# Kernel optimization log

Hardware: AMD Instinct MI355X
Metric: run time of the kernel (lower is better)

Reference implementation:

```python
import jax, jax.numpy as jnp
import numpy as np

B, N, K = 4, 1024, 4          # batch, nodes, neighbors-per-side (degree 2K)
FN, FE = 128, 64              # input node/edge feature dims
CN, CE = 128, 64              # output node/edge channels


def _build_graph():
    # degree-8 circulant graph; fixed edge count E = N*K
    A = np.zeros((N, N), np.float32)
    for d in range(1, K + 1):
        i = np.arange(N)
        A[i, (i + d) % N] = 1.0
        A[(i + d) % N, i] = 1.0
    # incidence matrix from upper-triangular nonzeros (row-major, as torch.nonzero)
    r, c = np.nonzero(np.triu(A))
    E = r.shape[0]
    inc = np.zeros((N, E), np.float32)
    ar = np.arange(E)
    inc[r, ar] = 1.0
    inc[c, ar] = 1.0

    def gcn_filter(M):
        Mh = M + np.eye(M.shape[0], dtype=np.float32)
        deg = Mh.sum(1)
        deg[deg == 0] = 1.0
        di = deg ** -0.5
        return (Mh * di[:, None]) * di[None, :]

    lap = gcn_filter(A)                                   # node GCN filter [N,N]
    line_adj = inc.T @ inc - 2.0 * np.eye(E, dtype=np.float32)  # line graph [E,E]
    edge_lap = gcn_filter(line_adj)                       # edge GCN filter [E,E]
    return lap, edge_lap, inc, E


def setup_inputs() -> dict:
    lap, edge_lap, inc, E = _build_graph()
    key = jax.random.key(0)
    ks = jax.random.split(key, 8)
    tile = lambda m: jnp.broadcast_to(jnp.asarray(m), (B,) + m.shape)
    return {
        "x": jax.random.normal(ks[0], (B, N, FN), jnp.float32),
        "e": jax.random.normal(ks[1], (B, E, FE), jnp.float32),
        "laplacian": tile(lap),
        "edge_laplacian": tile(edge_lap),
        "incidence": tile(inc),
        "node_kernel": jax.random.normal(ks[2], (FN, CN), jnp.float32) / np.sqrt(FN).astype(np.float32),
        "edge_kernel": jax.random.normal(ks[3], (FE, CE), jnp.float32) / np.sqrt(FE).astype(np.float32),
        "node_weights": jax.random.normal(ks[4], (FN, 1), jnp.float32) * 0.1,
        "edge_weights": jax.random.normal(ks[5], (FE, 1), jnp.float32) * 0.1,
        "node_bias": jax.random.uniform(ks[6], (CN,), jnp.float32, -0.05, 0.05),
        "edge_bias": jax.random.uniform(ks[7], (CE,), jnp.float32, -0.05, 0.05),
    }


def reference(x, e, laplacian, edge_laplacian, incidence, node_kernel, edge_kernel,
              node_weights, edge_weights, node_bias, edge_bias):
    # ---- node propagation: T diag(e @ ew) T^T * L_node, then @ x @ Wn ----
    we = jnp.einsum('bef,fo->be', e, edge_weights)  # [B,E], squeezed edge scores
    # incidence @ diag(we) @ incidence^T  == (incidence * we) @ incidence^T
    node_adj = jnp.matmul(incidence * we[:, None, :],
                          jnp.swapaxes(incidence, -1, -2)) * laplacian  # [B,N,N]
    node_out = jnp.matmul(jnp.matmul(node_adj, x), node_kernel) + node_bias
    node_out = jax.nn.relu(node_out)  # [B,N,CN]

    # ---- edge propagation: T^T diag(x @ nw) T * L_edge, then @ e @ We ----
    wn = jnp.einsum('bnf,fo->bn', x, node_weights)  # [B,N]
    inc_t = jnp.swapaxes(incidence, -1, -2)         # [B,E,N]
    edge_adj = jnp.matmul(inc_t * wn[:, None, :], incidence) * edge_laplacian  # [B,E,E]
    edge_out = jnp.matmul(jnp.matmul(edge_adj, e), edge_kernel) + edge_bias
    edge_out = jax.nn.relu(edge_out)  # [B,E,CE]

    return node_out, edge_out
```

## Files before the change

### kernel.cpp

```cpp
#include <hip/hip_runtime.h>

#define BB   4
#define NN   1024
#define EE   4096
#define FN_  128
#define FE_  64
#define CN_  128
#define CE_  64

typedef float f4 __attribute__((ext_vector_type(4)));

__device__ __forceinline__ float hsum(f4 a){
  return ((a[0] + a[1]) + a[2]) + a[3];
}

__device__ __forceinline__ int Soff(int r){
  if (r <= 3){ const int t[4] = {0, 8, 15, 21}; return t[r]; }
  if (r <= 1020) return 26 + 4*(r - 4);
  if (r == 1021) return 4093;
  if (r == 1022) return 4095;
  return 4096;
}

__device__ __forceinline__ void ep2uv(int ep, int& u, int& v){
  if (ep >= 4090){
    if      (ep <= 4092){ u = 1020; v = 1021 + (ep - 4090); }
    else if (ep <= 4094){ u = 1021; v = 1022 + (ep - 4093); }
    else                { u = 1022; v = 1023; }
  } else if (ep >= 26){
    u = 4 + (ep - 26) / 4;
    v = u + ((ep - 26) & 3) + 1;
  } else {
    const int r = (ep >= 21) ? 3 : (ep >= 15) ? 2 : (ep >= 8) ? 1 : 0;
    const int o = ep - Soff(r);
    u = r;
    v = (o < 4) ? (r + 1 + o) : (1020 + r + (o - 4));
  }
}

__device__ __forceinline__ void build_ninc(int n, int* a){
  int k = 0;
  for (int d = 4; d >= 1; --d){
    const int j = n - d;
    if (j >= 0) a[k++] = Soff(j) + (n - j - 1);
  }
  if (n >= 1020)
    for (int j = 0; j <= n - 1020; ++j)
      a[k++] = Soff(j) + 4 + (n - 1020 - j);
  const int cnt = (1023 - n) < 4 ? (1023 - n) : 4;
  for (int i = 0; i < cnt; ++i) a[k++] = Soff(n) + i;
  if (n <= 3)
    for (int i = 0; i <= 3 - n; ++i) a[k++] = Soff(n) + cnt + i;

  #pragma unroll
  for (int i2 = 1; i2 < 8; ++i2){
    int key = a[i2]; int j2 = i2 - 1;
    while (j2 >= 0 && a[j2] > key){ a[j2+1] = a[j2]; --j2; }
    a[j2+1] = key;
  }
}

__global__ __launch_bounds__(256) void k_all(
    const float* __restrict__ x, const float* __restrict__ e,
    const float* __restrict__ lap, const float* __restrict__ elap,
    const float* __restrict__ Wn, const float* __restrict__ We,
    const float* __restrict__ nb, const float* __restrict__ eb,
    const float* __restrict__ nw, const float* __restrict__ ew,
    float* __restrict__ node_out, float* __restrict__ edge_out)
{
  __shared__ int   sE[16][8];
  __shared__ float nWe[16][8];
  __shared__ float nCoef[16][8];
  __shared__ int   nJ[16][8];
  __shared__ float nDiag[16];
  __shared__ float yAll[16][FN_];
  __shared__ float ewL[FE_];
  __shared__ int   nlist[32][8];
  __shared__ int   sQ[16][16];
  __shared__ float sCoef[16][16];
  __shared__ int   sU[16], sV[16];
  __shared__ float sWnU[16], sWnV[16];
  __shared__ float zAll[16][CE_];

  const int tid = threadIdx.x;
  const int b   = blockIdx.y;

  if (blockIdx.x < NN/16){
    const int base = blockIdx.x * 16;
    if (tid < 16){
      ((f4*)ewL)[tid] = ((const f4*)ew)[tid];
      build_ninc(base + tid, sE[tid]);
    }
    __syncthreads();

    if (tid < 128){
      const int ii = tid >> 3, m = tid & 7;
      const int i  = base + ii;
      const int ep = sE[ii][m];
      const float* row = e + ((size_t)b*EE + ep) * FE_;
      f4 sv = {0.f, 0.f, 0.f, 0.f};
      #pragma unroll
      for (int t = 0; t < FE_/4; ++t)
        sv += *(const f4*)(row + t*4) * *(const f4*)(ewL + t*4);
      const float s = hsum(sv);
      int u, v2; ep2uv(ep, u, v2);
      const int j = u + v2 - i;
      nWe[ii][m]   = s;
      nJ[ii][m]    = j;
      nCoef[ii][m] = lap[(size_t)i*NN + j] * s;
    }
    __syncthreads();
    if (tid < 16){
      const int i = base + tid;
      float s = 0.f;
      #pragma unroll
      for (int m = 0; m < 8; ++m) s += nWe[tid][m];
      nDiag[tid] = lap[(size_t)i*NN + i] * s;
    }
    __syncthreads();

    {
      const int ii = tid >> 4, t = tid & 15;
      const float* xb = x + (size_t)b*NN*FN_;
      const float d = nDiag[ii];
      f4 y0 = d * *(const f4*)(xb + (size_t)(base + ii)*FN_ + t*8);
      f4 y1 = d * *(const f4*)(xb + (size_t)(base + ii)*FN_ + t*8 + 4);
      #pragma unroll
      for (int m = 0; m < 8; ++m){
        const float c = nCoef[ii][m];
        const float* xr = xb + (size_t)nJ[ii][m]*FN_ + t*8;
        y0 += c * *(const f4*)(xr);
        y1 += c * *(const f4*)(xr + 4);
      }
      *(f4*)(&yAll[ii][t*8])     = y0;
      *(f4*)(&yAll[ii][t*8 + 4]) = y1;
    }
    __syncthreads();

    const int half = tid >> 7;
    const int lane = tid & 127;
    f4 vacc[8];
    #pragma unroll
    for (int r = 0; r < 8; ++r) vacc[r] = (f4){0.f, 0.f, 0.f, 0.f};
    for (int f = 0; f < FN_; f += 4){
      const f4 w4 = { Wn[(f  )*CN_ + lane], Wn[(f+1)*CN_ + lane],
                      Wn[(f+2)*CN_ + lane], Wn[(f+3)*CN_ + lane] };
      #pragma unroll
      for (int r = 0; r < 8; ++r)
        vacc[r] += *(const f4*)(&yAll[half*8 + r][f]) * w4;
    }
    const float bv = nb[lane];
    #pragma unroll
    for (int r = 0; r < 8; ++r)
      node_out[((size_t)b*NN + base + half*8 + r)*CN_ + lane] =
          fmaxf(hsum(vacc[r]) + bv, 0.f);
  } else {
    const int base = (blockIdx.x - NN/16) * 16;
    if (tid < 16){
      int u, v; ep2uv(base + tid, u, v);
      sU[tid] = u; sV[tid] = v;
    }
    __syncthreads();

    if (tid < 32){
      const int node = (tid < 16) ? sU[tid] : sV[tid - 16];
      build_ninc(node, nlist[tid]);
    }
    {
      const int g = tid >> 3, h = tid & 7;
      const int node = (g < 16) ? sU[g] : sV[g - 16];
      const float* row = x + ((size_t)b*NN + node)*FN_ + h*16;
      f4 sv = {0.f, 0.f, 0.f, 0.f};
      #pragma unroll
      for (int t = 0; t < 4; ++t)
        sv += *(const f4*)(row + t*4) * *(const f4*)(nw + h*16 + t*4);
      float s = hsum(sv);
      s += __shfl_xor(s, 1); s += __shfl_xor(s, 2); s += __shfl_xor(s, 4);
      if (h == 0){ if (g < 16) sWnU[g] = s; else sWnV[g - 16] = s; }
    }
    __syncthreads();

    {
      const int pp = tid >> 4, k = tid & 15;
      const int p  = base + pp;
      const int q  = (k < 8) ? nlist[pp][k] : nlist[16 + pp][k - 8];
      const float ev = elap[(size_t)p*EE + q];
      float coef;
      if (q == p) coef = (k < 8) ? ev * (sWnU[pp] + sWnV[pp]) : 0.f;
      else        coef = ev * ((k < 8) ? sWnU[pp] : sWnV[pp]);
      sQ[pp][k]    = q;
      sCoef[pp][k] = coef;
    }
    __syncthreads();

    {
      const int pp = tid >> 4, t = tid & 15;
      const float* ebp = e + (size_t)b*EE*FE_;
      f4 z = {0.f, 0.f, 0.f, 0.f};
      #pragma unroll
      for (int k = 0; k < 16; ++k)
        z += sCoef[pp][k] * *(const f4*)(ebp + (size_t)sQ[pp][k]*FE_ + t*4);
      *(f4*)(&zAll[pp][t*4]) = z;
    }
    __syncthreads();

    const int grp  = tid >> 6;
    const int lane = tid & 63;
    f4 vacc[4];
    #pragma unroll
    for (int r = 0; r < 4; ++r) vacc[r] = (f4){0.f, 0.f, 0.f, 0.f};
    for (int f = 0; f < FE_; f += 4){
      const f4 w4 = { We[(f  )*CE_ + lane], We[(f+1)*CE_ + lane],
                      We[(f+2)*CE_ + lane], We[(f+3)*CE_ + lane] };
      #pragma unroll
      for (int r = 0; r < 4; ++r)
        vacc[r] += *(const f4*)(&zAll[grp*4 + r][f]) * w4;
    }
    const float bv = eb[lane];
    #pragma unroll
    for (int r = 0; r < 4; ++r)
      edge_out[((size_t)b*EE + base + grp*4 + r)*CE_ + lane] =
          fmaxf(hsum(vacc[r]) + bv, 0.f);
  }
}

extern "C" void kernel_launch(void* const* d_in, const int* in_sizes, int n_in,
                              void* d_out, int out_size, void* d_ws, size_t ws_size,
                              hipStream_t stream){
  const float* x    = (const float*)d_in[0];
  const float* e    = (const float*)d_in[1];
  const float* lap  = (const float*)d_in[2];
  const float* elap = (const float*)d_in[3];
  const float* Wn   = (const float*)d_in[5];
  const float* We   = (const float*)d_in[6];
  const float* nw   = (const float*)d_in[7];
  const float* ew   = (const float*)d_in[8];
  const float* nb   = (const float*)d_in[9];
  const float* eb   = (const float*)d_in[10];

  float* node_out = (float*)d_out;
  float* edge_out = (float*)d_out + (size_t)BB*NN*CN_;

  k_all<<<dim3(NN/16 + EE/16, BB), 256, 0, stream>>>(
      x, e, lap, elap, Wn, We, nb, eb, nw, ew, node_out, edge_out);
}
```

Before: 20.76 us.

## Fold batch into each block to share graph metadata and weight loads

Each block now handles all four batch elements instead of one batch index per grid row. Graph indices, Laplacian coefficients and weight loads are computed once and reused across batches, and node blocks cover 8 nodes instead of 16. Shared memory is unioned between the node and edge paths. The grid shrinks from 1280 to 384 blocks, which cuts redundant index and weight work but may lower parallelism and latency hiding on a large GPU.

```diff
diff --git a/kernel.cpp b/kernel.cpp
--- a/kernel.cpp
+++ b/kernel.cpp
@@ -7,6 +7,9 @@
 #define FE_  64
 #define CN_  128
 #define CE_  64
+
+#define NODE_NB 128
+#define EDGE_NB 256
 
 typedef float f4 __attribute__((ext_vector_type(4)));
 
@@ -60,6 +63,27 @@
   }
 }
 
+struct NodeSM {
+  int   sE[8][8];
+  int   nJ[8][8];
+  float lapv[8][8];
+  float lapd[8];
+  float nWe[4][8][8];
+  float nCoef[4][8][8];
+  float nDiag[4][8];
+  float ewL[FE_];
+  float yAll[4][8][FN_];
+};
+struct EdgeSM {
+  int   nlist[32][8];
+  int   nodeid[32];
+  int   sQ[16][16];
+  float elapv[16][16];
+  float sWn[4][32];
+  float sCoef[4][16][16];
+  float zAll[4][16][CE_];
+};
+
 __global__ __launch_bounds__(256) void k_all(
     const float* __restrict__ x, const float* __restrict__ e,
     const float* __restrict__ lap, const float* __restrict__ elap,
@@ -68,159 +92,177 @@
     const float* __restrict__ nw, const float* __restrict__ ew,
     float* __restrict__ node_out, float* __restrict__ edge_out)
 {
-  __shared__ int   sE[16][8];
-  __shared__ float nWe[16][8];
-  __shared__ float nCoef[16][8];
-  __shared__ int   nJ[16][8];
-  __shared__ float nDiag[16];
-  __shared__ float yAll[16][FN_];
-  __shared__ float ewL[FE_];
-  __shared__ int   nlist[32][8];
-  __shared__ int   sQ[16][16];
-  __shared__ float sCoef[16][16];
-  __shared__ int   sU[16], sV[16];
-  __shared__ float sWnU[16], sWnV[16];
-  __shared__ float zAll[16][CE_];
-
+  __shared__ union { NodeSM n; EdgeSM e; } sm;
   const int tid = threadIdx.x;
-  const int b   = blockIdx.y;
-
-  if (blockIdx.x < NN/16){
-    const int base = blockIdx.x * 16;
-    if (tid < 16){
-      ((f4*)ewL)[tid] = ((const f4*)ew)[tid];
-      build_ninc(base + tid, sE[tid]);
-    }
-    __syncthreads();
-
-    if (tid < 128){
+
+  if (blockIdx.x < NODE_NB){
+    const int base = blockIdx.x * 8;
+    if (tid < 16) ((f4*)sm.n.ewL)[tid] = ((const f4*)ew)[tid];
+    if (tid < 8)  build_ninc(base + tid, sm.n.sE[tid]);
+    __syncthreads();
+
+    if (tid < 64){
       const int ii = tid >> 3, m = tid & 7;
       const int i  = base + ii;
-      const int ep = sE[ii][m];
+      const int ep = sm.n.sE[ii][m];
+      int u, v; ep2uv(ep, u, v);
+      const int j = u + v - i;
+      sm.n.nJ[ii][m]   = j;
+      sm.n.lapv[ii][m] = lap[(size_t)i*NN + j];
+    } else if (tid < 72){
+      const int ii = tid - 64;
+      const int i  = base + ii;
+      sm.n.lapd[ii] = lap[(size_t)i*NN + i];
+    }
+    {
+      const int b = tid >> 6, ii = (tid >> 3) & 7, m = tid & 7;
+      const int ep = sm.n.sE[ii][m];
       const float* row = e + ((size_t)b*EE + ep) * FE_;
       f4 sv = {0.f, 0.f, 0.f, 0.f};
       #pragma unroll
       for (int t = 0; t < FE_/4; ++t)
-        sv += *(const f4*)(row + t*4) * *(const f4*)(ewL + t*4);
-      const float s = hsum(sv);
-      int u, v2; ep2uv(ep, u, v2);
-      const int j = u + v2 - i;
-      nWe[ii][m]   = s;
-      nJ[ii][m]    = j;
-      nCoef[ii][m] = lap[(size_t)i*NN + j] * s;
-    }
-    __syncthreads();
-    if (tid < 16){
-      const int i = base + tid;
+        sv += *(const f4*)(row + t*4) * *(const f4*)(sm.n.ewL + t*4);
+      sm.n.nWe[b][ii][m] = hsum(sv);
+    }
+    __syncthreads();
+
+    {
+      const int b = tid >> 6, ii = (tid >> 3) & 7, m = tid & 7;
+      sm.n.nCoef[b][ii][m] = sm.n.lapv[ii][m] * sm.n.nWe[b][ii][m];
+    }
+    if (tid < 32){
+      const int b = tid >> 3, ii = tid & 7;
       float s = 0.f;
       #pragma unroll
-      for (int m = 0; m < 8; ++m) s += nWe[tid][m];
-      nDiag[tid] = lap[(size_t)i*NN + i] * s;
-    }
-    __syncthreads();
-
-    {
-      const int ii = tid >> 4, t = tid & 15;
-      const float* xb = x + (size_t)b*NN*FN_;
-      const float d = nDiag[ii];
-      f4 y0 = d * *(const f4*)(xb + (size_t)(base + ii)*FN_ + t*8);
-      f4 y1 = d * *(const f4*)(xb + (size_t)(base + ii)*FN_ + t*8 + 4);
-      #pragma unroll
-      for (int m = 0; m < 8; ++m){
-        const float c = nCoef[ii][m];
-        const float* xr = xb + (size_t)nJ[ii][m]*FN_ + t*8;
-        y0 += c * *(const f4*)(xr);
-        y1 += c * *(const f4*)(xr + 4);
-      }
-      *(f4*)(&yAll[ii][t*8])     = y0;
-      *(f4*)(&yAll[ii][t*8 + 4]) = y1;
+      for (int m = 0; m < 8; ++m) s += sm.n.nWe[b][ii][m];
+      sm.n.nDiag[b][ii] = sm.n.lapd[ii] * s;
+    }
+    __syncthreads();
+
+    {
+      const int ii = tid >> 5, t = tid & 31;
+      #pragma unroll
+      for (int b = 0; b < 4; ++b){
+        const float* xb = x + (size_t)b*NN*FN_;
+        f4 y = sm.n.nDiag[b][ii] * *(const f4*)(xb + (size_t)(base + ii)*FN_ + t*4);
+        #pragma unroll
+        for (int m = 0; m < 8; ++m)
+          y += sm.n.nCoef[b][ii][m] * *(const f4*)(xb + (size_t)sm.n.nJ[ii][m]*FN_ + t*4);
+        *(f4*)(&sm.n.yAll[b][ii][t*4]) = y;
+      }
     }
     __syncthreads();
 
     const int half = tid >> 7;
     const int lane = tid & 127;
-    f4 vacc[8];
-    #pragma unroll
-    for (int r = 0; r < 8; ++r) vacc[r] = (f4){0.f, 0.f, 0.f, 0.f};
+    f4 vacc[4][4];
+    #pragma unroll
+    for (int b = 0; b < 4; ++b)
+      #pragma unroll
+      for (int r = 0; r < 4; ++r) vacc[b][r] = (f4){0.f, 0.f, 0.f, 0.f};
     for (int f = 0; f < FN_; f += 4){
       const f4 w4 = { Wn[(f  )*CN_ + lane], Wn[(f+1)*CN_ + lane],
                       Wn[(f+2)*CN_ + lane], Wn[(f+3)*CN_ + lane] };
       #pragma unroll
-      for (int r = 0; r < 8; ++r)
-        vacc[r] += *(const f4*)(&yAll[half*8 + r][f]) * w4;
+      for (int b = 0; b < 4; ++b)
+        #pragma unroll
+        for (int r = 0; r < 4; ++r)
+          vacc[b][r] += *(const f4*)(&sm.n.yAll[b][half*4 + r][f]) * w4;
     }
     const float bv = nb[lane];
     #pragma unroll
-    for (int r = 0; r < 8; ++r)
-      node_out[((size_t)b*NN + base + half*8 + r)*CN_ + lane] =
-          fmaxf(hsum(vacc[r]) + bv, 0.f);
+    for (int b = 0; b < 4; ++b)
+      #pragma unroll
+      for (int r = 0; r < 4; ++r)
+        node_out[((size_t)b*NN + base + half*4 + r)*CN_ + lane] =
+            fmaxf(hsum(vacc[b][r]) + bv, 0.f);
   } else {
-    const int base = (blockIdx.x - NN/16) * 16;
-    if (tid < 16){
-      int u, v; ep2uv(base + tid, u, v);
-      sU[tid] = u; sV[tid] = v;
-    }
-    __syncthreads();
-
+    const int base = (blockIdx.x - NODE_NB) * 16;
     if (tid < 32){
-      const int node = (tid < 16) ? sU[tid] : sV[tid - 16];
-      build_ninc(node, nlist[tid]);
-    }
-    {
-      const int g = tid >> 3, h = tid & 7;
-      const int node = (g < 16) ? sU[g] : sV[g - 16];
-      const float* row = x + ((size_t)b*NN + node)*FN_ + h*16;
-      f4 sv = {0.f, 0.f, 0.f, 0.f};
-      #pragma unroll
-      for (int t = 0; t < 4; ++t)
-        sv += *(const f4*)(row + t*4) * *(const f4*)(nw + h*16 + t*4);
-      float s = hsum(sv);
-      s += __shfl_xor(s, 1); s += __shfl_xor(s, 2); s += __shfl_xor(s, 4);
-      if (h == 0){ if (g < 16) sWnU[g] = s; else sWnV[g - 16] = s; }
+      int u, v; ep2uv(base + (tid & 15), u, v);
+      const int node = (tid < 16) ? u : v;
+      sm.e.nodeid[tid] = node;
+      build_ninc(node, sm.e.nlist[tid]);
     }
     __syncthreads();
 
     {
       const int pp = tid >> 4, k = tid & 15;
       const int p  = base + pp;
-      const int q  = (k < 8) ? nlist[pp][k] : nlist[16 + pp][k - 8];
-      const float ev = elap[(size_t)p*EE + q];
-      float coef;
-      if (q == p) coef = (k < 8) ? ev * (sWnU[pp] + sWnV[pp]) : 0.f;
-      else        coef = ev * ((k < 8) ? sWnU[pp] : sWnV[pp]);
-      sQ[pp][k]    = q;
-      sCoef[pp][k] = coef;
+      const int q  = (k < 8) ? sm.e.nlist[pp][k] : sm.e.nlist[16 + pp][k - 8];
+      sm.e.sQ[pp][k]    = q;
+      sm.e.elapv[pp][k] = elap[(size_t)p*EE + q];
+    }
+    if (tid < 128){
+      const int g = tid & 31, b = tid >> 5;
+      const float* row = x + ((size_t)b*NN + sm.e.nodeid[g]) * FN_;
+      float part[8];
+      #pragma unroll
+      for (int h = 0; h < 8; ++h){
+        f4 sv = {0.f, 0.f, 0.f, 0.f};
+        #pragma unroll
+        for (int t = 0; t < 4; ++t)
+          sv += *(const f4*)(row + h*16 + t*4) * *(const f4*)(nw + h*16 + t*4);
+        part[h] = hsum(sv);
+      }
+      sm.e.sWn[b][g] = ((part[0] + part[1]) + (part[2] + part[3]))
+                     + ((part[4] + part[5]) + (part[6] + part[7]));
+    }
+    __syncthreads();
+
+    {
+      const int pp = tid >> 4, k = tid & 15;
+      const int p  = base + pp;
+      const int q  = sm.e.sQ[pp][k];
+      const float ev = sm.e.elapv[pp][k];
+      #pragma unroll
+      for (int b = 0; b < 4; ++b){
+        const float wu = sm.e.sWn[b][pp], wv = sm.e.sWn[b][16 + pp];
+        float coef;
+        if (q == p) coef = (k < 8) ? ev * (wu + wv) : 0.f;
+        else        coef = ev * ((k < 8) ? wu : wv);
+        sm.e.sCoef[b][pp][k] = coef;
+      }
     }
     __syncthreads();
 
     {
       const int pp = tid >> 4, t = tid & 15;
-      const float* ebp = e + (size_t)b*EE*FE_;
-      f4 z = {0.f, 0.f, 0.f, 0.f};
-      #pragma unroll
-      for (int k = 0; k < 16; ++k)
-        z += sCoef[pp][k] * *(const f4*)(ebp + (size_t)sQ[pp][k]*FE_ + t*4);
-      *(f4*)(&zAll[pp][t*4]) = z;
+      #pragma unroll
+      for (int b = 0; b < 4; ++b){
+        const float* ebp = e + (size_t)b*EE*FE_;
+        f4 z = {0.f, 0.f, 0.f, 0.f};
+        #pragma unroll
+        for (int k = 0; k < 16; ++k)
+          z += sm.e.sCoef[b][pp][k] * *(const f4*)(ebp + (size_t)sm.e.sQ[pp][k]*FE_ + t*4);
+        *(f4*)(&sm.e.zAll[b][pp][t*4]) = z;
+      }
     }
     __syncthreads();
 
     const int grp  = tid >> 6;
     const int lane = tid & 63;
-    f4 vacc[4];
-    #pragma unroll
-    for (int r = 0; r < 4; ++r) vacc[r] = (f4){0.f, 0.f, 0.f, 0.f};
+    f4 vacc[4][4];
+    #pragma unroll
+    for (int b = 0; b < 4; ++b)
+      #pragma unroll
+      for (int r = 0; r < 4; ++r) vacc[b][r] = (f4){0.f, 0.f, 0.f, 0.f};
     for (int f = 0; f < FE_; f += 4){
       const f4 w4 = { We[(f  )*CE_ + lane], We[(f+1)*CE_ + lane],
                       We[(f+2)*CE_ + lane], We[(f+3)*CE_ + lane] };
       #pragma unroll
+      for (int b = 0; b < 4; ++b)
+        #pragma unroll
+        for (int r = 0; r < 4; ++r)
+          vacc[b][r] += *(const f4*)(&sm.e.zAll[b][grp*4 + r][f]) * w4;
+    }
+    const float bv = eb[lane];
+    #pragma unroll
+    for (int b = 0; b < 4; ++b)
+      #pragma unroll
       for (int r = 0; r < 4; ++r)
-        vacc[r] += *(const f4*)(&zAll[grp*4 + r][f]) * w4;
-    }
-    const float bv = eb[lane];
-    #pragma unroll
-    for (int r = 0; r < 4; ++r)
-      edge_out[((size_t)b*EE + base + grp*4 + r)*CE_ + lane] =
-          fmaxf(hsum(vacc[r]) + bv, 0.f);
+        edge_out[((size_t)b*EE + base + grp*4 + r)*CE_ + lane] =
+            fmaxf(hsum(vacc[b][r]) + bv, 0.f);
   }
 }
 
@@ -241,6 +283,6 @@
   float* node_out = (float*)d_out;
   float* edge_out = (float*)d_out + (size_t)BB*NN*CN_;
 
-  k_all<<<dim3(NN/16 + EE/16, BB), 256, 0, stream>>>(
+  k_all<<<NODE_NB + EDGE_NB, 256, 0, stream>>>(
       x, e, lap, elap, Wn, We, nb, eb, nw, ew, node_out, edge_out);
 }
```

Result: slower. 28.77 us (+38.6%).

## Halve node rows per block, union shared memory, parallelize diagonal laplacian loads

Applied to the files above, without the earlier changes.

Node blocks now handle 8 nodes instead of 16, which doubles the node-block count to 128 per batch and gives better load balance against the heavier edge blocks. Node and edge shared-memory buffers are placed in a union to cut per-block LDS usage and allow higher occupancy. The diagonal laplacian loads are issued by otherwise idle threads in parallel with the edge-score phase. The tradeoff is that each node block amortizes its Wn reads over fewer rows, so total Wn traffic goes up.

```diff
diff --git a/kernel.cpp b/kernel.cpp
--- a/kernel.cpp
+++ b/kernel.cpp
@@ -7,6 +7,9 @@
 #define FE_  64
 #define CN_  128
 #define CE_  64
+
+#define NODE_NB 128
+#define EDGE_NB 256
 
 typedef float f4 __attribute__((ext_vector_type(4)));
 
@@ -60,6 +63,25 @@
   }
 }
 
+struct NodeSM {
+  int   sE[8][8];
+  int   nJ[8][8];
+  float lapd[8];
+  float nWe[8][8];
+  float nCoef[8][8];
+  float nDiag[8];
+  float ewL[FE_];
+  float yAll[8][FN_];
+};
+struct EdgeSM {
+  int   nlist[32][8];
+  int   sQ[16][16];
+  float sCoef[16][16];
+  int   sU[16], sV[16];
+  float sWnU[16], sWnV[16];
+  float zAll[16][CE_];
+};
+
 __global__ __launch_bounds__(256) void k_all(
     const float* __restrict__ x, const float* __restrict__ e,
     const float* __restrict__ lap, const float* __restrict__ elap,
@@ -68,107 +90,88 @@
     const float* __restrict__ nw, const float* __restrict__ ew,
     float* __restrict__ node_out, float* __restrict__ edge_out)
 {
-  __shared__ int   sE[16][8];
-  __shared__ float nWe[16][8];
-  __shared__ float nCoef[16][8];
-  __shared__ int   nJ[16][8];
-  __shared__ float nDiag[16];
-  __shared__ float yAll[16][FN_];
-  __shared__ float ewL[FE_];
-  __shared__ int   nlist[32][8];
-  __shared__ int   sQ[16][16];
-  __shared__ float sCoef[16][16];
-  __shared__ int   sU[16], sV[16];
-  __shared__ float sWnU[16], sWnV[16];
-  __shared__ float zAll[16][CE_];
-
+  __shared__ union { NodeSM n; EdgeSM e; } sm;
   const int tid = threadIdx.x;
   const int b   = blockIdx.y;
 
-  if (blockIdx.x < NN/16){
-    const int base = blockIdx.x * 16;
-    if (tid < 16){
-      ((f4*)ewL)[tid] = ((const f4*)ew)[tid];
-      build_ninc(base + tid, sE[tid]);
-    }
-    __syncthreads();
-
-    if (tid < 128){
+  if (blockIdx.x < NODE_NB){
+    const int base = blockIdx.x * 8;
+    if (tid < 16) ((f4*)sm.n.ewL)[tid] = ((const f4*)ew)[tid];
+    if (tid < 8)  build_ninc(base + tid, sm.n.sE[tid]);
+    __syncthreads();
+
+    if (tid < 64){
       const int ii = tid >> 3, m = tid & 7;
       const int i  = base + ii;
-      const int ep = sE[ii][m];
+      const int ep = sm.n.sE[ii][m];
       const float* row = e + ((size_t)b*EE + ep) * FE_;
       f4 sv = {0.f, 0.f, 0.f, 0.f};
       #pragma unroll
       for (int t = 0; t < FE_/4; ++t)
-        sv += *(const f4*)(row + t*4) * *(const f4*)(ewL + t*4);
+        sv += *(const f4*)(row + t*4) * *(const f4*)(sm.n.ewL + t*4);
       const float s = hsum(sv);
       int u, v2; ep2uv(ep, u, v2);
       const int j = u + v2 - i;
-      nWe[ii][m]   = s;
-      nJ[ii][m]    = j;
-      nCoef[ii][m] = lap[(size_t)i*NN + j] * s;
-    }
-    __syncthreads();
-    if (tid < 16){
-      const int i = base + tid;
+      sm.n.nWe[ii][m]   = s;
+      sm.n.nJ[ii][m]    = j;
+      sm.n.nCoef[ii][m] = lap[(size_t)i*NN + j] * s;
+    } else if (tid < 72){
+      const int ii = tid - 64;
+      const int i  = base + ii;
+      sm.n.lapd[ii] = lap[(size_t)i*NN + i];
+    }
+    __syncthreads();
+    if (tid < 8){
       float s = 0.f;
       #pragma unroll
-      for (int m = 0; m < 8; ++m) s += nWe[tid][m];
-      nDiag[tid] = lap[(size_t)i*NN + i] * s;
-    }
-    __syncthreads();
-
-    {
-      const int ii = tid >> 4, t = tid & 15;
+      for (int m = 0; m < 8; ++m) s += sm.n.nWe[tid][m];
+      sm.n.nDiag[tid] = sm.n.lapd[tid] * s;
+    }
+    __syncthreads();
+
+    {
+      const int ii = tid >> 5, t = tid & 31;
       const float* xb = x + (size_t)b*NN*FN_;
-      const float d = nDiag[ii];
-      f4 y0 = d * *(const f4*)(xb + (size_t)(base + ii)*FN_ + t*8);
-      f4 y1 = d * *(const f4*)(xb + (size_t)(base + ii)*FN_ + t*8 + 4);
-      #pragma unroll
-      for (int m = 0; m < 8; ++m){
-        const float c = nCoef[ii][m];
-        const float* xr = xb + (size_t)nJ[ii][m]*FN_ + t*8;
-        y0 += c * *(const f4*)(xr);
-        y1 += c * *(const f4*)(xr + 4);
-      }
-      *(f4*)(&yAll[ii][t*8])     = y0;
-      *(f4*)(&yAll[ii][t*8 + 4]) = y1;
+      f4 y = sm.n.nDiag[ii] * *(const f4*)(xb + (size_t)(base + ii)*FN_ + t*4);
+      #pragma unroll
+      for (int m = 0; m < 8; ++m)
+        y += sm.n.nCoef[ii][m] * *(const f4*)(xb + (size_t)sm.n.nJ[ii][m]*FN_ + t*4);
+      *(f4*)(&sm.n.yAll[ii][t*4]) = y;
     }
     __syncthreads();
 
     const int half = tid >> 7;
     const int lane = tid & 127;
-    f4 vacc[8];
-    #pragma unroll
-    for (int r = 0; r < 8; ++r) vacc[r] = (f4){0.f, 0.f, 0.f, 0.f};
+    f4 vacc[4];
+    #pragma unroll
+    for (int r = 0; r < 4; ++r) vacc[r] = (f4){0.f, 0.f, 0.f, 0.f};
     for (int f = 0; f < FN_; f += 4){
       const f4 w4 = { Wn[(f  )*CN_ + lane], Wn[(f+1)*CN_ + lane],
                       Wn[(f+2)*CN_ + lane], Wn[(f+3)*CN_ + lane] };
       #pragma unroll
-      for (int r = 0; r < 8; ++r)
-        vacc[r] += *(const f4*)(&yAll[half*8 + r][f]) * w4;
+      for (int r = 0; r < 4; ++r)
+        vacc[r] += *(const f4*)(&sm.n.yAll[half*4 + r][f]) * w4;
     }
     const float bv = nb[lane];
     #pragma unroll
-    for (int r = 0; r < 8; ++r)
-      node_out[((size_t)b*NN + base + half*8 + r)*CN_ + lane] =
+    for (int r = 0; r < 4; ++r)
+      node_out[((size_t)b*NN + base + half*4 + r)*CN_ + lane] =
           fmaxf(hsum(vacc[r]) + bv, 0.f);
   } else {
-    const int base = (blockIdx.x - NN/16) * 16;
+    const int base = (blockIdx.x - NODE_NB) * 16;
     if (tid < 16){
       int u, v; ep2uv(base + tid, u, v);
-      sU[tid] = u; sV[tid] = v;
+      sm.e.sU[tid] = u; sm.e.sV[tid] = v;
     }
     __syncthreads();
 
     if (tid < 32){
-      const int node = (tid < 16) ? sU[tid] : sV[tid - 16];
-      build_ninc(node, nlist[tid]);
+      const int node = (tid < 16) ? sm.e.sU[tid] : sm.e.sV[tid - 16];
+      build_ninc(node, sm.e.nlist[tid]);
     }
     {
       const int g = tid >> 3, h = tid & 7;
-      const int node = (g < 16) ? sU[g] : sV[g - 16];
+      const int node = (g < 16) ? sm.e.sU[g] : sm.e.sV[g - 16];
       const float* row = x + ((size_t)b*NN + node)*FN_ + h*16;
       f4 sv = {0.f, 0.f, 0.f, 0.f};
       #pragma unroll
@@ -176,20 +179,20 @@
         sv += *(const f4*)(row + t*4) * *(const f4*)(nw + h*16 + t*4);
       float s = hsum(sv);
       s += __shfl_xor(s, 1); s += __shfl_xor(s, 2); s += __shfl_xor(s, 4);
-      if (h == 0){ if (g < 16) sWnU[g] = s; else sWnV[g - 16] = s; }
+      if (h == 0){ if (g < 16) sm.e.sWnU[g] = s; else sm.e.sWnV[g - 16] = s; }
     }
     __syncthreads();
 
     {
       const int pp = tid >> 4, k = tid & 15;
       const int p  = base + pp;
-      const int q  = (k < 8) ? nlist[pp][k] : nlist[16 + pp][k - 8];
+      const int q  = (k < 8) ? sm.e.nlist[pp][k] : sm.e.nlist[16 + pp][k - 8];
       const float ev = elap[(size_t)p*EE + q];
       float coef;
-      if (q == p) coef = (k < 8) ? ev * (sWnU[pp] + sWnV[pp]) : 0.f;
-      else        coef = ev * ((k < 8) ? sWnU[pp] : sWnV[pp]);
-      sQ[pp][k]    = q;
-      sCoef[pp][k] = coef;
+      if (q == p) coef = (k < 8) ? ev * (sm.e.sWnU[pp] + sm.e.sWnV[pp]) : 0.f;
+      else        coef = ev * ((k < 8) ? sm.e.sWnU[pp] : sm.e.sWnV[pp]);
+      sm.e.sQ[pp][k]    = q;
+      sm.e.sCoef[pp][k] = coef;
     }
     __syncthreads();
 
@@ -199,8 +202,8 @@
       f4 z = {0.f, 0.f, 0.f, 0.f};
       #pragma unroll
       for (int k = 0; k < 16; ++k)
-        z += sCoef[pp][k] * *(const f4*)(ebp + (size_t)sQ[pp][k]*FE_ + t*4);
-      *(f4*)(&zAll[pp][t*4]) = z;
+        z += sm.e.sCoef[pp][k] * *(const f4*)(ebp + (size_t)sm.e.sQ[pp][k]*FE_ + t*4);
+      *(f4*)(&sm.e.zAll[pp][t*4]) = z;
     }
     __syncthreads();
 
@@ -214,7 +217,7 @@
                       We[(f+2)*CE_ + lane], We[(f+3)*CE_ + lane] };
       #pragma unroll
       for (int r = 0; r < 4; ++r)
-        vacc[r] += *(const f4*)(&zAll[grp*4 + r][f]) * w4;
+        vacc[r] += *(const f4*)(&sm.e.zAll[grp*4 + r][f]) * w4;
     }
     const float bv = eb[lane];
     #pragma unroll
@@ -241,6 +244,6 @@
   float* node_out = (float*)d_out;
   float* edge_out = (float*)d_out + (size_t)BB*NN*CN_;
 
-  k_all<<<dim3(NN/16 + EE/16, BB), 256, 0, stream>>>(
+  k_all<<<dim3(NODE_NB + EDGE_NB, BB), 256, 0, stream>>>(
       x, e, lap, elap, Wn, We, nb, eb, nw, ew, node_out, edge_out);
 }
```

Measured after the change: 23.75 us. 1.14x slower.
